# Optimization experiments

Measured on AMD Instinct MI355X. Metric: run time of the kernel, lower is better.

The kernel has to match this reference:

```python
import jax, jax.numpy as jnp
import numpy as np

N, M, D = 1024, 32, 512


def setup_inputs() -> dict:
    key = jax.random.key(0)
    k1, = jax.random.split(key, 1)
    emb = jax.random.normal(k1, (N, M, D), dtype=jnp.float32)
    emb = emb / jnp.linalg.norm(emb, axis=-1, keepdims=True)  # module expects normed embeddings
    return {
        "normed_embedding": emb,
        "n": N,
        "m": M,
        "ln_w": jnp.array(10.0, dtype=jnp.float32),
        "ln_b": jnp.array(-5.0, dtype=jnp.float32),
    }


def reference(normed_embedding, n, m, ln_w, ln_b):
    # normed_embedding: [N, M, D]
    ck = jnp.mean(normed_embedding, axis=1)          # [N, D] inclusive centroids
    sums = jnp.sum(normed_embedding, axis=1)         # [N, D]
    e = normed_embedding.reshape(n * m, -1)          # [NM, D]
    sims = jnp.matmul(e, ck.T)                       # [NM, N]

    # exclusive centroid for own speaker: cj = (sum_i - e_ij) / (m - 1)
    ex = jnp.sum(normed_embedding * (sums[:, None, :] - normed_embedding), axis=-1) / (m - 1)  # [N, M]
    rows = jnp.arange(n * m)
    spk = rows // m                                  # speaker label per row
    sims = sims.at[rows, spk].set(ex.reshape(-1))

    sims = jax.nn.sigmoid(ln_w * sims + ln_b)

    own = sims[rows, spk]                            # [NM]
    own_col = spk[:, None] == jnp.arange(n)[None, :]  # mask own speaker column
    max_other = jnp.max(jnp.where(own_col, -jnp.inf, sims), axis=-1)  # [NM]
    loss = jnp.mean(1.0 - own + max_other).reshape(1)

    preds = jnp.argmax(sims, axis=1)
    batch_acc = jnp.mean((preds == spk).astype(jnp.float32))
    return loss, batch_acc
```

## Files before the change

kernel.cpp:

```cpp
#include <hip/hip_runtime.h>


#define N_SPK 1024
#define M_UTT 32
#define D_DIM 512
#define NROWS (N_SPK * M_UTT)
#define BM 256
#define BN 256
#define NTILES (N_SPK / BN)
#define MTILES (NROWS / BM)
#define NWG (MTILES * NTILES)

typedef __attribute__((ext_vector_type(8))) short short8v;
typedef __attribute__((ext_vector_type(4))) float f32x4;

__device__ __forceinline__ unsigned short f2bf(float f) {
    union { float f; unsigned int u; } v; v.f = f;
    unsigned int u = v.u;
    u += 0x7fffu + ((u >> 16) & 1u);
    return (unsigned short)(u >> 16);
}

__device__ __forceinline__ void gload_lds16(const void* g, void* l) {
    __builtin_amdgcn_global_load_lds(
        (const __attribute__((address_space(1))) unsigned int*)g,
        (__attribute__((address_space(3))) unsigned int*)l, 16, 0, 0);
}

__device__ __forceinline__ float sigmoidf(float x) {
    return 1.f / (1.f + __expf(-x));
}

template <int MH, int NH>
__device__ __forceinline__ void qmm(f32x4 (&acc)[8][4],
                                    const short8v (&a)[4][2],
                                    const short8v (&b)[2][2]) {
#pragma unroll
    for (int mf = 0; mf < 4; ++mf)
#pragma unroll
        for (int nf = 0; nf < 2; ++nf) {
            acc[MH * 4 + mf][NH * 2 + nf] = __builtin_amdgcn_mfma_f32_16x16x32_bf16(
                a[mf][0], b[nf][0], acc[MH * 4 + mf][NH * 2 + nf], 0, 0, 0);
            acc[MH * 4 + mf][NH * 2 + nf] = __builtin_amdgcn_mfma_f32_16x16x32_bf16(
                a[mf][1], b[nf][1], acc[MH * 4 + mf][NH * 2 + nf], 0, 0, 0);
        }
}

__global__ void __launch_bounds__(256) prep_kernel(const float* __restrict__ emb,
                                                   const float* __restrict__ lnw,
                                                   unsigned short* __restrict__ ebf,
                                                   unsigned short* __restrict__ ck) {
    __shared__ float part[2][D_DIM];
    const int n = blockIdx.x;
    const int t = threadIdx.x;
    const int d4 = (t & 127) * 4;
    const int mh = t >> 7;
    const float* base = emb + (size_t)n * M_UTT * D_DIM;
    unsigned short* obase = ebf + (size_t)n * M_UTT * D_DIM;

    float4 acc = {0.f, 0.f, 0.f, 0.f};
#pragma unroll
    for (int mm = 0; mm < 16; ++mm) {
        const int m = mh * 16 + mm;
        const float4 v = *reinterpret_cast<const float4*>(base + m * D_DIM + d4);
        acc.x += v.x; acc.y += v.y; acc.z += v.z; acc.w += v.w;
        ushort4 b;
        b.x = f2bf(v.x); b.y = f2bf(v.y); b.z = f2bf(v.z); b.w = f2bf(v.w);
        *reinterpret_cast<ushort4*>(obase + m * D_DIM + d4) = b;
    }
    *reinterpret_cast<float4*>(&part[mh][d4]) = acc;
    __syncthreads();
    if (t < 128) {
        const float sgn = (lnw[0] >= 0.f) ? 1.f : -1.f;
        const float sc = sgn * (1.f / 32.f);
        const int d = t * 4;
        const float4 a = *reinterpret_cast<const float4*>(&part[0][d]);
        const float4 b = *reinterpret_cast<const float4*>(&part[1][d]);
        ushort4 o;
        o.x = f2bf((a.x + b.x) * sc); o.y = f2bf((a.y + b.y) * sc);
        o.z = f2bf((a.z + b.z) * sc); o.w = f2bf((a.w + b.w) * sc);
        *reinterpret_cast<ushort4*>(ck + (size_t)n * D_DIM + d) = o;
    }
}

__global__ void __launch_bounds__(512, 2)
gemm_kernel(const unsigned short* __restrict__ ebf,
            const unsigned short* __restrict__ ck,
            float* __restrict__ maxo_part,
            float* __restrict__ own_part) {
    __shared__ __align__(16) unsigned short ring[2][32768];

    const int tid  = threadIdx.x;
    const int lane = tid & 63;
    const int wv   = tid >> 6;
    const int lo   = lane & 15;
    const int hi   = lane >> 4;
    const int wm   = wv >> 2;
    const int wn   = wv & 3;

    const int raw   = blockIdx.x;
    const int xcd   = raw & 7;
    const int local = raw >> 3;
    const int mt    = xcd * 16 + (local >> 2);
    const int nt    = local & 3;
    const int r0    = mt * BM;
    const int n0    = nt * BN;

    const unsigned short* pA[2];
    const unsigned short* pB[2];
    int doff[2];
#pragma unroll
    for (int j = 0; j < 2; ++j) {
        const int s   = j * 512 + tid;
        const int row = s >> 3;
        const int l   = (s & 7) ^ (row & 7);
        pA[j] = ebf + (size_t)(r0 + row) * D_DIM + l * 8;
        pB[j] = ck  + (size_t)(n0 + row) * D_DIM + l * 8;
        doff[j] = s * 8;
    }

    auto stage_h = [&](int tile, int h) {
        unsigned short* dst = &ring[tile & 1][0];
        const int off = tile * 64 + h * (128 * D_DIM);
#pragma unroll
        for (int j = 0; j < 2; ++j) {
            gload_lds16(pA[j] + off, dst + h * 8192 + doff[j]);
            gload_lds16(pB[j] + off, dst + 16384 + h * 8192 + doff[j]);
        }
    };

    stage_h(0, 0);
    stage_h(0, 1);
    stage_h(1, 0);
    asm volatile("s_waitcnt vmcnt(4)" ::: "memory");
    __builtin_amdgcn_s_barrier();
    __builtin_amdgcn_sched_barrier(0);

    const int ph0   = (hi ^ (lo & 7)) * 16;
    const int ph1   = ((4 + hi) ^ (lo & 7)) * 16;
    const int arow0 = (wm * 128 + lo) * 128;
    const int bcol0 = 32768 + (wn * 64 + lo) * 128;

    f32x4 acc[8][4];
#pragma unroll
    for (int am = 0; am < 8; ++am)
#pragma unroll
        for (int an = 0; an < 4; ++an) acc[am][an] = (f32x4){0.f, 0.f, 0.f, 0.f};

    short8v a[4][2], b0c[2][2], b1c[2][2];

    for (int t = 0; t < 8; ++t) {
        const char* bufp = (const char*)&ring[t & 1][0];

#pragma unroll
        for (int mf = 0; mf < 4; ++mf) {
            a[mf][0] = *reinterpret_cast<const short8v*>(bufp + arow0 + mf * 2048 + ph0);
            a[mf][1] = *reinterpret_cast<const short8v*>(bufp + arow0 + mf * 2048 + ph1);
        }
#pragma unroll
        for (int nf = 0; nf < 2; ++nf) {
            b0c[nf][0] = *reinterpret_cast<const short8v*>(bufp + bcol0 + nf * 2048 + ph0);
            b0c[nf][1] = *reinterpret_cast<const short8v*>(bufp + bcol0 + nf * 2048 + ph1);
        }
        if (t < 7) stage_h(t + 1, 1);
        __builtin_amdgcn_s_barrier();
        __builtin_amdgcn_s_setprio(1);
        qmm<0, 0>(acc, a, b0c);
        __builtin_amdgcn_s_setprio(0);
        __builtin_amdgcn_s_barrier();

#pragma unroll
        for (int nf = 0; nf < 2; ++nf) {
            b1c[nf][0] = *reinterpret_cast<const short8v*>(bufp + bcol0 + 4096 + nf * 2048 + ph0);
            b1c[nf][1] = *reinterpret_cast<const short8v*>(bufp + bcol0 + 4096 + nf * 2048 + ph1);
        }
        __builtin_amdgcn_s_barrier();
        __builtin_amdgcn_s_setprio(1);
        qmm<0, 1>(acc, a, b1c);
        __builtin_amdgcn_s_setprio(0);
        __builtin_amdgcn_s_barrier();

#pragma unroll
        for (int mf = 0; mf < 4; ++mf) {
            a[mf][0] = *reinterpret_cast<const short8v*>(bufp + arow0 + 8192 + mf * 2048 + ph0);
            a[mf][1] = *reinterpret_cast<const short8v*>(bufp + arow0 + 8192 + mf * 2048 + ph1);
        }
        __builtin_amdgcn_s_barrier();
        __builtin_amdgcn_s_setprio(1);
        qmm<1, 1>(acc, a, b1c);
        __builtin_amdgcn_s_setprio(0);
        __builtin_amdgcn_s_barrier();

        if (t < 6) stage_h(t + 2, 0);
        __builtin_amdgcn_s_barrier();
        __builtin_amdgcn_s_setprio(1);
        qmm<1, 0>(acc, a, b0c);
        __builtin_amdgcn_s_setprio(0);
        if (t < 6)       asm volatile("s_waitcnt vmcnt(4)" ::: "memory");
        else if (t == 6) asm volatile("s_waitcnt vmcnt(0)" ::: "memory");
        __builtin_amdgcn_s_barrier();
        __builtin_amdgcn_sched_barrier(0);
    }

    __syncthreads();
    float* red = (float*)&ring[0][0];
    const float NEG = -1e30f;

#pragma unroll
    for (int am = 0; am < 8; ++am) {
#pragma unroll
        for (int reg = 0; reg < 4; ++reg) {
            const int rl   = wm * 128 + am * 16 + hi * 4 + reg;
            const int rowg = r0 + rl;
            const int spk  = rowg >> 5;
            float m = NEG, o = NEG;
#pragma unroll
            for (int an = 0; an < 4; ++an) {
                const int col = n0 + wn * 64 + an * 16 + lo;
                const float v = acc[am][an][reg];
                const bool dg = (col == spk);
                o = dg ? v : o;
                m = fmaxf(m, dg ? NEG : v);
            }
#pragma unroll
            for (int mask = 1; mask < 16; mask <<= 1) {
                m = fmaxf(m, __shfl_xor(m, mask));
                o = fmaxf(o, __shfl_xor(o, mask));
            }
            if (lo == 0) {
                red[wn * 256 + rl]        = m;
                red[1024 + wn * 256 + rl] = o;
            }
        }
    }
    __syncthreads();

    if (tid < 256) {
        const float mo = fmaxf(fmaxf(red[tid], red[256 + tid]),
                               fmaxf(red[512 + tid], red[768 + tid]));
        maxo_part[(size_t)nt * NROWS + r0 + tid] = mo;
        if (nt == (mt >> 5)) {
            const float op = fmaxf(fmaxf(red[1024 + tid], red[1280 + tid]),
                                   fmaxf(red[1536 + tid], red[1792 + tid]));
            own_part[r0 + tid] = op;
        }
    }
}

__global__ void __launch_bounds__(256) rowred_kernel(const float* __restrict__ maxo_part,
                                                     const float* __restrict__ own_part,
                                                     const float* __restrict__ lnw,
                                                     const float* __restrict__ lnb,
                                                     float* __restrict__ partsum) {
    const int r = blockIdx.x * 256 + threadIdx.x;
    const float lw = lnw[0], lb = lnb[0];
    const float sgn = (lw >= 0.f) ? 1.f : -1.f;
    const float alw = fabsf(lw);

    float mo = maxo_part[r];
#pragma unroll
    for (int nt2 = 1; nt2 < NTILES; ++nt2)
        mo = fmaxf(mo, maxo_part[(size_t)nt2 * NROWS + r]);
    const float ownp  = own_part[r];
    const float s_own = sgn * ownp;
    const float ex    = (32.f * s_own - 1.f) * (1.f / 31.f);
    const float own_s = sigmoidf(lw * ex + lb);
    const float mo_s  = sigmoidf(alw * mo + lb);
    float loss = 1.f - own_s + mo_s;
    float corr = (sgn * ex >= mo) ? 1.f : 0.f;

#pragma unroll
    for (int mask = 1; mask < 64; mask <<= 1) {
        loss += __shfl_xor(loss, mask);
        corr += __shfl_xor(corr, mask);
    }
    __shared__ float sl[4], sc[4];
    const int wv = threadIdx.x >> 6;
    if ((threadIdx.x & 63) == 0) { sl[wv] = loss; sc[wv] = corr; }
    __syncthreads();
    if (threadIdx.x == 0) {
        partsum[blockIdx.x]       = sl[0] + sl[1] + sl[2] + sl[3];
        partsum[128 + blockIdx.x] = sc[0] + sc[1] + sc[2] + sc[3];
    }
}

__global__ void __launch_bounds__(128) final_kernel(const float* __restrict__ partsum,
                                                    float* __restrict__ out) {
    const int t = threadIdx.x;
    float l = partsum[t];
    float c = partsum[128 + t];
#pragma unroll
    for (int mask = 1; mask < 64; mask <<= 1) {
        l += __shfl_xor(l, mask);
        c += __shfl_xor(c, mask);
    }
    __shared__ float sl[2], sc[2];
    if ((t & 63) == 0) { sl[t >> 6] = l; sc[t >> 6] = c; }
    __syncthreads();
    if (t == 0) {
        out[0] = (sl[0] + sl[1]) * (1.f / (float)NROWS);
        out[1] = (sc[0] + sc[1]) * (1.f / (float)NROWS);
    }
}

extern "C" void kernel_launch(void* const* d_in, const int* in_sizes, int n_in,
                              void* d_out, int out_size, void* d_ws, size_t ws_size,
                              hipStream_t stream) {
    (void)in_sizes; (void)n_in; (void)out_size; (void)ws_size;
    const float* emb = (const float*)d_in[0];
    const float* lnw = (const float*)d_in[3];
    const float* lnb = (const float*)d_in[4];
    float* out = (float*)d_out;

    char* ws = (char*)d_ws;
    unsigned short* ebf = (unsigned short*)ws;
    unsigned short* ck  = (unsigned short*)(ws + (size_t)NROWS * D_DIM * 2);
    float* maxo_part = (float*)(ws + (size_t)NROWS * D_DIM * 2
                                   + (size_t)N_SPK * D_DIM * 2);
    float* own_part  = (float*)((char*)maxo_part + (size_t)NTILES * NROWS * 4);
    float* partsum   = (float*)((char*)own_part + (size_t)NROWS * 4);

    prep_kernel<<<N_SPK, 256, 0, stream>>>(emb, lnw, ebf, ck);
    gemm_kernel<<<NWG, 512, 0, stream>>>(ebf, ck, maxo_part, own_part);
    rowred_kernel<<<NROWS / 256, 256, 0, stream>>>(maxo_part, own_part, lnw, lnb, partsum);
    final_kernel<<<1, 128, 0, stream>>>(partsum, out);
}
```

Measured before the change: 66.36 us.

## Fuse bf16 conversion of embeddings into GEMM loader and process two row panels per block

The prep kernel no longer writes a bf16 copy of the embeddings. The GEMM now loads fp32 embeddings through registers, truncates them to bf16, and stores them into LDS. Each workgroup covers 512 rows as two 256-row panels, keeping the centroid B tiles streamed, with half as many workgroups. This removes the extra global write and reread of the bf16 copy, at the cost of register-staged loads, more VALU packing work, fewer blocks (256 on the device), and truncation instead of round-to-nearest for A.

After: 81.93 us. 1.23x slower.

```diff
diff --git a/kernel.cpp b/kernel.cpp
--- a/kernel.cpp
+++ b/kernel.cpp
@@ -5,14 +5,12 @@
 #define M_UTT 32
 #define D_DIM 512
 #define NROWS (N_SPK * M_UTT)
-#define BM 256
-#define BN 256
-#define NTILES (N_SPK / BN)
-#define MTILES (NROWS / BM)
-#define NWG (MTILES * NTILES)
+#define NTILES 4
+#define GRID_G 256
 
 typedef __attribute__((ext_vector_type(8))) short short8v;
 typedef __attribute__((ext_vector_type(4))) float f32x4;
+typedef __attribute__((ext_vector_type(4))) unsigned int u32x4;
 
 __device__ __forceinline__ unsigned short f2bf(float f) {
     union { float f; unsigned int u; } v; v.f = f;
@@ -21,6 +19,11 @@
     return (unsigned short)(u >> 16);
 }
 
+__device__ __forceinline__ unsigned int pk2(float a, float b) {
+    union { float f; unsigned int u; } ua, ub; ua.f = a; ub.f = b;
+    return (ub.u & 0xFFFF0000u) | (ua.u >> 16);
+}
+
 __device__ __forceinline__ void gload_lds16(const void* g, void* l) {
     __builtin_amdgcn_global_load_lds(
         (const __attribute__((address_space(1))) unsigned int*)g,
@@ -46,17 +49,15 @@
         }
 }
 
-__global__ void __launch_bounds__(256) prep_kernel(const float* __restrict__ emb,
-                                                   const float* __restrict__ lnw,
-                                                   unsigned short* __restrict__ ebf,
-                                                   unsigned short* __restrict__ ck) {
+__global__ void __launch_bounds__(256) ck_kernel(const float* __restrict__ emb,
+                                                 const float* __restrict__ lnw,
+                                                 unsigned short* __restrict__ ck) {
     __shared__ float part[2][D_DIM];
     const int n = blockIdx.x;
     const int t = threadIdx.x;
     const int d4 = (t & 127) * 4;
     const int mh = t >> 7;
     const float* base = emb + (size_t)n * M_UTT * D_DIM;
-    unsigned short* obase = ebf + (size_t)n * M_UTT * D_DIM;
 
     float4 acc = {0.f, 0.f, 0.f, 0.f};
 #pragma unroll
@@ -64,9 +65,6 @@
         const int m = mh * 16 + mm;
         const float4 v = *reinterpret_cast<const float4*>(base + m * D_DIM + d4);
         acc.x += v.x; acc.y += v.y; acc.z += v.z; acc.w += v.w;
-        ushort4 b;
-        b.x = f2bf(v.x); b.y = f2bf(v.y); b.z = f2bf(v.z); b.w = f2bf(v.w);
-        *reinterpret_cast<ushort4*>(obase + m * D_DIM + d4) = b;
     }
     *reinterpret_cast<float4*>(&part[mh][d4]) = acc;
     __syncthreads();
@@ -84,11 +82,12 @@
 }
 
 __global__ void __launch_bounds__(512, 2)
-gemm_kernel(const unsigned short* __restrict__ ebf,
+gemm_kernel(const float* __restrict__ emb,
             const unsigned short* __restrict__ ck,
             float* __restrict__ maxo_part,
             float* __restrict__ own_part) {
-    __shared__ __align__(16) unsigned short ring[2][32768];
+    __shared__ __align__(16) unsigned short buf[2][32768];
+    __shared__ float red[2][2][4][256];
 
     const int tid  = threadIdx.x;
     const int lane = tid & 63;
@@ -99,150 +98,206 @@
     const int wn   = wv & 3;
 
     const int raw   = blockIdx.x;
-    const int xcd   = raw & 7;
-    const int local = raw >> 3;
-    const int mt    = xcd * 16 + (local >> 2);
-    const int nt    = local & 3;
-    const int r0    = mt * BM;
-    const int n0    = nt * BN;
-
-    const unsigned short* pA[2];
-    const unsigned short* pB[2];
-    int doff[2];
+    const int P     = (raw & 7) * 8 + ((raw >> 3) >> 2);
+    const int ntb   = (raw >> 3) & 3;
+    const int r0    = P * 512;
+    const int n0    = ntb * 256;
+
+    const int lsw = (tid & 7) ^ ((tid >> 3) & 7);
+    const unsigned aoff0 = (unsigned)(r0 + (tid >> 3)) * 512u + (unsigned)lsw * 8u;
+    const unsigned boff0 = (unsigned)(n0 + (tid >> 3)) * 512u + (unsigned)lsw * 8u;
+    const int dA = tid * 8;
+    const int dB = 16384 + tid * 8;
+
+    const int ph0   = (hi ^ (lo & 7)) * 8;
+    const int ph1   = ((4 + hi) ^ (lo & 7)) * 8;
+    const int abase = (wm * 128 + lo) * 64;
+    const int bbase = 16384 + (wn * 64 + lo) * 64;
+
+    float4 ga[4], gb[4];
+
 #pragma unroll
     for (int j = 0; j < 2; ++j) {
-        const int s   = j * 512 + tid;
-        const int row = s >> 3;
-        const int l   = (s & 7) ^ (row & 7);
-        pA[j] = ebf + (size_t)(r0 + row) * D_DIM + l * 8;
-        pB[j] = ck  + (size_t)(n0 + row) * D_DIM + l * 8;
-        doff[j] = s * 8;
-    }
-
-    auto stage_h = [&](int tile, int h) {
-        unsigned short* dst = &ring[tile & 1][0];
-        const int off = tile * 64 + h * (128 * D_DIM);
-#pragma unroll
-        for (int j = 0; j < 2; ++j) {
-            gload_lds16(pA[j] + off, dst + h * 8192 + doff[j]);
-            gload_lds16(pB[j] + off, dst + 16384 + h * 8192 + doff[j]);
-        }
-    };
-
-    stage_h(0, 0);
-    stage_h(0, 1);
-    stage_h(1, 0);
+        ga[2 * j]     = *reinterpret_cast<const float4*>(emb + aoff0 + j * 32768u);
+        ga[2 * j + 1] = *reinterpret_cast<const float4*>(emb + aoff0 + j * 32768u + 4u);
+        gb[2 * j]     = *reinterpret_cast<const float4*>(emb + aoff0 + (j + 2) * 32768u);
+        gb[2 * j + 1] = *reinterpret_cast<const float4*>(emb + aoff0 + (j + 2) * 32768u + 4u);
+    }
+#pragma unroll
+    for (int j = 0; j < 4; ++j)
+        gload_lds16(ck + boff0 + j * 32768u, &buf[0][dB + j * 4096]);
+#pragma unroll
+    for (int j = 0; j < 4; ++j)
+        gload_lds16(ck + boff0 + j * 32768u + 64u, &buf[1][dB + j * 4096]);
+    {
+        u32x4 w0 = {pk2(ga[0].x, ga[0].y), pk2(ga[0].z, ga[0].w),
+                    pk2(ga[1].x, ga[1].y), pk2(ga[1].z, ga[1].w)};
+        u32x4 w1 = {pk2(ga[2].x, ga[2].y), pk2(ga[2].z, ga[2].w),
+                    pk2(ga[3].x, ga[3].y), pk2(ga[3].z, ga[3].w)};
+        u32x4 w2 = {pk2(gb[0].x, gb[0].y), pk2(gb[0].z, gb[0].w),
+                    pk2(gb[1].x, gb[1].y), pk2(gb[1].z, gb[1].w)};
+        u32x4 w3 = {pk2(gb[2].x, gb[2].y), pk2(gb[2].z, gb[2].w),
+                    pk2(gb[3].x, gb[3].y), pk2(gb[3].z, gb[3].w)};
+        *reinterpret_cast<u32x4*>(&buf[0][dA])         = w0;
+        *reinterpret_cast<u32x4*>(&buf[0][dA + 4096])  = w1;
+        *reinterpret_cast<u32x4*>(&buf[0][dA + 8192])  = w2;
+        *reinterpret_cast<u32x4*>(&buf[0][dA + 12288]) = w3;
+    }
+    asm volatile("s_waitcnt lgkmcnt(0)" ::: "memory");
     asm volatile("s_waitcnt vmcnt(4)" ::: "memory");
     __builtin_amdgcn_s_barrier();
     __builtin_amdgcn_sched_barrier(0);
 
-    const int ph0   = (hi ^ (lo & 7)) * 16;
-    const int ph1   = ((4 + hi) ^ (lo & 7)) * 16;
-    const int arow0 = (wm * 128 + lo) * 128;
-    const int bcol0 = 32768 + (wn * 64 + lo) * 128;
-
     f32x4 acc[8][4];
 #pragma unroll
     for (int am = 0; am < 8; ++am)
 #pragma unroll
         for (int an = 0; an < 4; ++an) acc[am][an] = (f32x4){0.f, 0.f, 0.f, 0.f};
 
-    short8v a[4][2], b0c[2][2], b1c[2][2];
-
-    for (int t = 0; t < 8; ++t) {
-        const char* bufp = (const char*)&ring[t & 1][0];
-
+    short8v afr[4][2], b0c[2][2], b1c[2][2];
+    const float NEG = -1e30f;
+
+#pragma unroll
+    for (int tau = 0; tau < 16; ++tau) {
+        const int cur = tau & 1;
+        const unsigned short* bp  = &buf[cur][0];
+        unsigned short*       bpn = &buf[cur ^ 1][0];
+        const unsigned kA = (unsigned)((((tau + 1) >> 3) * 131072) + (((tau + 1) & 7) * 64));
+        const unsigned kB = (unsigned)(((tau + 2) & 7) * 64);
+
+        if (tau < 15) {
+#pragma unroll
+            for (int j = 0; j < 2; ++j) {
+                ga[2 * j]     = *reinterpret_cast<const float4*>(emb + aoff0 + kA + j * 32768u);
+                ga[2 * j + 1] = *reinterpret_cast<const float4*>(emb + aoff0 + kA + j * 32768u + 4u);
+            }
+        }
 #pragma unroll
         for (int mf = 0; mf < 4; ++mf) {
-            a[mf][0] = *reinterpret_cast<const short8v*>(bufp + arow0 + mf * 2048 + ph0);
-            a[mf][1] = *reinterpret_cast<const short8v*>(bufp + arow0 + mf * 2048 + ph1);
+            afr[mf][0] = *reinterpret_cast<const short8v*>(bp + abase + mf * 1024 + ph0);
+            afr[mf][1] = *reinterpret_cast<const short8v*>(bp + abase + mf * 1024 + ph1);
         }
 #pragma unroll
         for (int nf = 0; nf < 2; ++nf) {
-            b0c[nf][0] = *reinterpret_cast<const short8v*>(bufp + bcol0 + nf * 2048 + ph0);
-            b0c[nf][1] = *reinterpret_cast<const short8v*>(bufp + bcol0 + nf * 2048 + ph1);
-        }
-        if (t < 7) stage_h(t + 1, 1);
+            b0c[nf][0] = *reinterpret_cast<const short8v*>(bp + bbase + nf * 1024 + ph0);
+            b0c[nf][1] = *reinterpret_cast<const short8v*>(bp + bbase + nf * 1024 + ph1);
+        }
         __builtin_amdgcn_s_barrier();
         __builtin_amdgcn_s_setprio(1);
-        qmm<0, 0>(acc, a, b0c);
+        qmm<0, 0>(acc, afr, b0c);
         __builtin_amdgcn_s_setprio(0);
         __builtin_amdgcn_s_barrier();
 
+        if (tau < 15) {
+#pragma unroll
+            for (int j = 0; j < 2; ++j) {
+                gb[2 * j]     = *reinterpret_cast<const float4*>(emb + aoff0 + kA + (j + 2) * 32768u);
+                gb[2 * j + 1] = *reinterpret_cast<const float4*>(emb + aoff0 + kA + (j + 2) * 32768u + 4u);
+            }
+        }
 #pragma unroll
         for (int nf = 0; nf < 2; ++nf) {
-            b1c[nf][0] = *reinterpret_cast<const short8v*>(bufp + bcol0 + 4096 + nf * 2048 + ph0);
-            b1c[nf][1] = *reinterpret_cast<const short8v*>(bufp + bcol0 + 4096 + nf * 2048 + ph1);
+            b1c[nf][0] = *reinterpret_cast<const short8v*>(bp + bbase + 2048 + nf * 1024 + ph0);
+            b1c[nf][1] = *reinterpret_cast<const short8v*>(bp + bbase + 2048 + nf * 1024 + ph1);
         }
         __builtin_amdgcn_s_barrier();
         __builtin_amdgcn_s_setprio(1);
-        qmm<0, 1>(acc, a, b1c);
+        qmm<0, 1>(acc, afr, b1c);
         __builtin_amdgcn_s_setprio(0);
         __builtin_amdgcn_s_barrier();
 
+        if (tau < 14) {
+#pragma unroll
+            for (int j = 0; j < 4; ++j)
+                gload_lds16(ck + boff0 + kB + j * 32768u, &buf[cur][dB + j * 4096]);
+        }
+        if (tau < 15) {
+            u32x4 w0 = {pk2(ga[0].x, ga[0].y), pk2(ga[0].z, ga[0].w),
+                        pk2(ga[1].x, ga[1].y), pk2(ga[1].z, ga[1].w)};
+            u32x4 w1 = {pk2(ga[2].x, ga[2].y), pk2(ga[2].z, ga[2].w),
+                        pk2(ga[3].x, ga[3].y), pk2(ga[3].z, ga[3].w)};
+            *reinterpret_cast<u32x4*>(bpn + dA)        = w0;
+            *reinterpret_cast<u32x4*>(bpn + dA + 4096) = w1;
+        }
 #pragma unroll
         for (int mf = 0; mf < 4; ++mf) {
-            a[mf][0] = *reinterpret_cast<const short8v*>(bufp + arow0 + 8192 + mf * 2048 + ph0);
-            a[mf][1] = *reinterpret_cast<const short8v*>(bufp + arow0 + 8192 + mf * 2048 + ph1);
+            afr[mf][0] = *reinterpret_cast<const short8v*>(bp + abase + 4096 + mf * 1024 + ph0);
+            afr[mf][1] = *reinterpret_cast<const short8v*>(bp + abase + 4096 + mf * 1024 + ph1);
         }
         __builtin_amdgcn_s_barrier();
         __builtin_amdgcn_s_setprio(1);
-        qmm<1, 1>(acc, a, b1c);
+        qmm<1, 1>(acc, afr, b1c);
         __builtin_amdgcn_s_setprio(0);
         __builtin_amdgcn_s_barrier();
 
-        if (t < 6) stage_h(t + 2, 0);
+        if (tau < 15) {
+            u32x4 w2 = {pk2(gb[0].x, gb[0].y), pk2(gb[0].z, gb[0].w),
+                        pk2(gb[1].x, gb[1].y), pk2(gb[1].z, gb[1].w)};
+            u32x4 w3 = {pk2(gb[2].x, gb[2].y), pk2(gb[2].z, gb[2].w),
+                        pk2(gb[3].x, gb[3].y), pk2(gb[3].z, gb[3].w)};
+            *reinterpret_cast<u32x4*>(bpn + dA + 8192)  = w2;
+            *reinterpret_cast<u32x4*>(bpn + dA + 12288) = w3;
+        }
+        asm volatile("s_waitcnt lgkmcnt(0)" ::: "memory");
         __builtin_amdgcn_s_barrier();
         __builtin_amdgcn_s_setprio(1);
-        qmm<1, 0>(acc, a, b0c);
+        qmm<1, 0>(acc, afr, b0c);
         __builtin_amdgcn_s_setprio(0);
-        if (t < 6)       asm volatile("s_waitcnt vmcnt(4)" ::: "memory");
-        else if (t == 6) asm volatile("s_waitcnt vmcnt(0)" ::: "memory");
         __builtin_amdgcn_s_barrier();
         __builtin_amdgcn_sched_barrier(0);
+
+        if (tau == 7 || tau == 15) {
+            const int pan = tau >> 3;
+#pragma unroll
+            for (int am = 0; am < 8; ++am) {
+#pragma unroll
+                for (int reg = 0; reg < 4; ++reg) {
+                    const int rl   = wm * 128 + am * 16 + hi * 4 + reg;
+                    const int rowg = r0 + pan * 256 + rl;
+                    const int spk  = rowg >> 5;
+                    float m = NEG, o = NEG;
+#pragma unroll
+                    for (int an = 0; an < 4; ++an) {
+                        const int col = n0 + wn * 64 + an * 16 + lo;
+                        const float v = acc[am][an][reg];
+                        const bool dg = (col == spk);
+                        o = dg ? v : o;
+                        m = fmaxf(m, dg ? NEG : v);
+                    }
+#pragma unroll
+                    for (int mask = 1; mask < 16; mask <<= 1) {
+                        m = fmaxf(m, __shfl_xor(m, mask));
+                        o = fmaxf(o, __shfl_xor(o, mask));
+                    }
+                    if (lo == 0) {
+                        red[pan][0][wn][rl] = m;
+                        red[pan][1][wn][rl] = o;
+                    }
+                }
+            }
+            if (tau == 7) {
+#pragma unroll
+                for (int am = 0; am < 8; ++am)
+#pragma unroll
+                    for (int an = 0; an < 4; ++an)
+                        acc[am][an] = (f32x4){0.f, 0.f, 0.f, 0.f};
+            }
+        }
     }
 
     __syncthreads();
-    float* red = (float*)&ring[0][0];
-    const float NEG = -1e30f;
-
-#pragma unroll
-    for (int am = 0; am < 8; ++am) {
-#pragma unroll
-        for (int reg = 0; reg < 4; ++reg) {
-            const int rl   = wm * 128 + am * 16 + hi * 4 + reg;
-            const int rowg = r0 + rl;
-            const int spk  = rowg >> 5;
-            float m = NEG, o = NEG;
-#pragma unroll
-            for (int an = 0; an < 4; ++an) {
-                const int col = n0 + wn * 64 + an * 16 + lo;
-                const float v = acc[am][an][reg];
-                const bool dg = (col == spk);
-                o = dg ? v : o;
-                m = fmaxf(m, dg ? NEG : v);
-            }
-#pragma unroll
-            for (int mask = 1; mask < 16; mask <<= 1) {
-                m = fmaxf(m, __shfl_xor(m, mask));
-                o = fmaxf(o, __shfl_xor(o, mask));
-            }
-            if (lo == 0) {
-                red[wn * 256 + rl]        = m;
-                red[1024 + wn * 256 + rl] = o;
-            }
-        }
-    }
-    __syncthreads();
-
     if (tid < 256) {
-        const float mo = fmaxf(fmaxf(red[tid], red[256 + tid]),
-                               fmaxf(red[512 + tid], red[768 + tid]));
-        maxo_part[(size_t)nt * NROWS + r0 + tid] = mo;
-        if (nt == (mt >> 5)) {
-            const float op = fmaxf(fmaxf(red[1024 + tid], red[1280 + tid]),
-                                   fmaxf(red[1536 + tid], red[1792 + tid]));
-            own_part[r0 + tid] = op;
+#pragma unroll
+        for (int pan = 0; pan < 2; ++pan) {
+            const float mo = fmaxf(fmaxf(red[pan][0][0][tid], red[pan][0][1][tid]),
+                                   fmaxf(red[pan][0][2][tid], red[pan][0][3][tid]));
+            maxo_part[(size_t)ntb * NROWS + r0 + pan * 256 + tid] = mo;
+            const int mtp = P * 2 + pan;
+            if (ntb == (mtp >> 5)) {
+                const float op = fmaxf(fmaxf(red[pan][1][0][tid], red[pan][1][1][tid]),
+                                       fmaxf(red[pan][1][2][tid], red[pan][1][3][tid]));
+                own_part[r0 + pan * 256 + tid] = op;
+            }
         }
     }
 }
@@ -313,15 +368,13 @@
     float* out = (float*)d_out;
 
     char* ws = (char*)d_ws;
-    unsigned short* ebf = (unsigned short*)ws;
-    unsigned short* ck  = (unsigned short*)(ws + (size_t)NROWS * D_DIM * 2);
-    float* maxo_part = (float*)(ws + (size_t)NROWS * D_DIM * 2
-                                   + (size_t)N_SPK * D_DIM * 2);
+    unsigned short* ck = (unsigned short*)ws;
+    float* maxo_part = (float*)(ws + (size_t)N_SPK * D_DIM * 2);
     float* own_part  = (float*)((char*)maxo_part + (size_t)NTILES * NROWS * 4);
     float* partsum   = (float*)((char*)own_part + (size_t)NROWS * 4);
 
-    prep_kernel<<<N_SPK, 256, 0, stream>>>(emb, lnw, ebf, ck);
-    gemm_kernel<<<NWG, 512, 0, stream>>>(ebf, ck, maxo_part, own_part);
+    ck_kernel<<<N_SPK, 256, 0, stream>>>(emb, lnw, ck);
+    gemm_kernel<<<GRID_G, 512, 0, stream>>>(emb, ck, maxo_part, own_part);
     rowred_kernel<<<NROWS / 256, 256, 0, stream>>>(maxo_part, own_part, lnw, lnb, partsum);
     final_kernel<<<1, 128, 0, stream>>>(partsum, out);
 }
```

## Make GEMM workgroups sweep two column tiles, halving grid and partials

Applied to the files above, without the earlier changes.

Each GEMM workgroup now walks two consecutive 256-column speaker tiles (16 K-steps in one pipelined loop) instead of one. Row max and own-speaker values are folded into registers at each tile boundary and the accumulators reset. The grid drops from 512 to 256 workgroups, so each A row-tile is loaded by two workgroups instead of four and only two maxo partials go to rowred. The cost is extra register pressure from the mx/ow arrays and the fully unrolled loop, plus fewer workgroups to fill the CUs (256 CUs on MI355X, one wave of launches).

After: 82.75 us. +24.7%, slower.

```diff
diff --git a/kernel.cpp b/kernel.cpp
--- a/kernel.cpp
+++ b/kernel.cpp
@@ -6,10 +6,9 @@
 #define D_DIM 512
 #define NROWS (N_SPK * M_UTT)
 #define BM 256
-#define BN 256
-#define NTILES (N_SPK / BN)
-#define MTILES (NROWS / BM)
-#define NWG (MTILES * NTILES)
+#define NPARTS 2
+#define GRID_G 256
+#define NKT 16
 
 typedef __attribute__((ext_vector_type(8))) short short8v;
 typedef __attribute__((ext_vector_type(4))) float f32x4;
@@ -101,10 +100,10 @@
     const int raw   = blockIdx.x;
     const int xcd   = raw & 7;
     const int local = raw >> 3;
-    const int mt    = xcd * 16 + (local >> 2);
-    const int nt    = local & 3;
+    const int mt    = xcd * 16 + (local & 15);
+    const int ch    = local >> 4;
     const int r0    = mt * BM;
-    const int n0    = nt * BN;
+    const int c0    = ch * 512;
 
     const unsigned short* pA[2];
     const unsigned short* pB[2];
@@ -115,17 +114,18 @@
         const int row = s >> 3;
         const int l   = (s & 7) ^ (row & 7);
         pA[j] = ebf + (size_t)(r0 + row) * D_DIM + l * 8;
-        pB[j] = ck  + (size_t)(n0 + row) * D_DIM + l * 8;
+        pB[j] = ck  + (size_t)(c0 + row) * D_DIM + l * 8;
         doff[j] = s * 8;
     }
 
     auto stage_h = [&](int tile, int h) {
         unsigned short* dst = &ring[tile & 1][0];
-        const int off = tile * 64 + h * (128 * D_DIM);
+        const int offA = (tile & 7) * 64 + h * (128 * D_DIM);
+        const int offB = offA + ((tile >> 3) << 17);
 #pragma unroll
         for (int j = 0; j < 2; ++j) {
-            gload_lds16(pA[j] + off, dst + h * 8192 + doff[j]);
-            gload_lds16(pB[j] + off, dst + 16384 + h * 8192 + doff[j]);
+            gload_lds16(pA[j] + offA, dst + h * 8192 + doff[j]);
+            gload_lds16(pB[j] + offB, dst + 16384 + h * 8192 + doff[j]);
         }
     };
 
@@ -142,14 +142,21 @@
     const int bcol0 = 32768 + (wn * 64 + lo) * 128;
 
     f32x4 acc[8][4];
+    float mx[8][4], ow[8][4];
+    const float NEG = -1e30f;
 #pragma unroll
     for (int am = 0; am < 8; ++am)
 #pragma unroll
         for (int an = 0; an < 4; ++an) acc[am][an] = (f32x4){0.f, 0.f, 0.f, 0.f};
+#pragma unroll
+    for (int am = 0; am < 8; ++am)
+#pragma unroll
+        for (int reg = 0; reg < 4; ++reg) { mx[am][reg] = NEG; ow[am][reg] = NEG; }
 
     short8v a[4][2], b0c[2][2], b1c[2][2];
 
-    for (int t = 0; t < 8; ++t) {
+#pragma unroll
+    for (int t = 0; t < NKT; ++t) {
         const char* bufp = (const char*)&ring[t & 1][0];
 
 #pragma unroll
@@ -162,7 +169,7 @@
             b0c[nf][0] = *reinterpret_cast<const short8v*>(bufp + bcol0 + nf * 2048 + ph0);
             b0c[nf][1] = *reinterpret_cast<const short8v*>(bufp + bcol0 + nf * 2048 + ph1);
         }
-        if (t < 7) stage_h(t + 1, 1);
+        if (t < NKT - 1) stage_h(t + 1, 1);
         __builtin_amdgcn_s_barrier();
         __builtin_amdgcn_s_setprio(1);
         qmm<0, 0>(acc, a, b0c);
@@ -191,43 +198,58 @@
         __builtin_amdgcn_s_setprio(0);
         __builtin_amdgcn_s_barrier();
 
-        if (t < 6) stage_h(t + 2, 0);
+        if (t < NKT - 2) stage_h(t + 2, 0);
         __builtin_amdgcn_s_barrier();
         __builtin_amdgcn_s_setprio(1);
         qmm<1, 0>(acc, a, b0c);
         __builtin_amdgcn_s_setprio(0);
-        if (t < 6)       asm volatile("s_waitcnt vmcnt(4)" ::: "memory");
-        else if (t == 6) asm volatile("s_waitcnt vmcnt(0)" ::: "memory");
+        if (t < NKT - 2)       asm volatile("s_waitcnt vmcnt(4)" ::: "memory");
+        else if (t == NKT - 2) asm volatile("s_waitcnt vmcnt(0)" ::: "memory");
         __builtin_amdgcn_s_barrier();
         __builtin_amdgcn_sched_barrier(0);
+
+        if (t == 7 || t == 15) {
+            const int ntl = t >> 3;
+#pragma unroll
+            for (int am = 0; am < 8; ++am)
+#pragma unroll
+                for (int reg = 0; reg < 4; ++reg) {
+                    const int rowg = r0 + wm * 128 + am * 16 + hi * 4 + reg;
+                    const int spk  = rowg >> 5;
+#pragma unroll
+                    for (int an = 0; an < 4; ++an) {
+                        const int col = c0 + ntl * 256 + wn * 64 + an * 16 + lo;
+                        const float v = acc[am][an][reg];
+                        const bool dg = (col == spk);
+                        ow[am][reg] = dg ? v : ow[am][reg];
+                        mx[am][reg] = fmaxf(mx[am][reg], dg ? NEG : v);
+                    }
+                }
+            if (t == 7) {
+#pragma unroll
+                for (int am = 0; am < 8; ++am)
+#pragma unroll
+                    for (int an = 0; an < 4; ++an)
+                        acc[am][an] = (f32x4){0.f, 0.f, 0.f, 0.f};
+            }
+        }
     }
 
     __syncthreads();
     float* red = (float*)&ring[0][0];
-    const float NEG = -1e30f;
 
 #pragma unroll
     for (int am = 0; am < 8; ++am) {
 #pragma unroll
         for (int reg = 0; reg < 4; ++reg) {
-            const int rl   = wm * 128 + am * 16 + hi * 4 + reg;
-            const int rowg = r0 + rl;
-            const int spk  = rowg >> 5;
-            float m = NEG, o = NEG;
-#pragma unroll
-            for (int an = 0; an < 4; ++an) {
-                const int col = n0 + wn * 64 + an * 16 + lo;
-                const float v = acc[am][an][reg];
-                const bool dg = (col == spk);
-                o = dg ? v : o;
-                m = fmaxf(m, dg ? NEG : v);
-            }
+            float m = mx[am][reg], o = ow[am][reg];
 #pragma unroll
             for (int mask = 1; mask < 16; mask <<= 1) {
                 m = fmaxf(m, __shfl_xor(m, mask));
                 o = fmaxf(o, __shfl_xor(o, mask));
             }
             if (lo == 0) {
+                const int rl = wm * 128 + am * 16 + hi * 4 + reg;
                 red[wn * 256 + rl]        = m;
                 red[1024 + wn * 256 + rl] = o;
             }
@@ -238,8 +260,8 @@
     if (tid < 256) {
         const float mo = fmaxf(fmaxf(red[tid], red[256 + tid]),
                                fmaxf(red[512 + tid], red[768 + tid]));
-        maxo_part[(size_t)nt * NROWS + r0 + tid] = mo;
-        if (nt == (mt >> 5)) {
+        maxo_part[(size_t)ch * NROWS + r0 + tid] = mo;
+        if (ch == (mt >> 6)) {
             const float op = fmaxf(fmaxf(red[1024 + tid], red[1280 + tid]),
                                    fmaxf(red[1536 + tid], red[1792 + tid]));
             own_part[r0 + tid] = op;
@@ -257,10 +279,7 @@
     const float sgn = (lw >= 0.f) ? 1.f : -1.f;
     const float alw = fabsf(lw);
 
-    float mo = maxo_part[r];
-#pragma unroll
-    for (int nt2 = 1; nt2 < NTILES; ++nt2)
-        mo = fmaxf(mo, maxo_part[(size_t)nt2 * NROWS + r]);
+    const float mo = fmaxf(maxo_part[r], maxo_part[(size_t)NROWS + r]);
     const float ownp  = own_part[r];
     const float s_own = sgn * ownp;
     const float ex    = (32.f * s_own - 1.f) * (1.f / 31.f);
@@ -317,11 +336,11 @@
     unsigned short* ck  = (unsigned short*)(ws + (size_t)NROWS * D_DIM * 2);
     float* maxo_part = (float*)(ws + (size_t)NROWS * D_DIM * 2
                                    + (size_t)N_SPK * D_DIM * 2);
-    float* own_part  = (float*)((char*)maxo_part + (size_t)NTILES * NROWS * 4);
+    float* own_part  = (float*)((char*)maxo_part + (size_t)NPARTS * NROWS * 4);
     float* partsum   = (float*)((char*)own_part + (size_t)NROWS * 4);
 
     prep_kernel<<<N_SPK, 256, 0, stream>>>(emb, lnw, ebf, ck);
-    gemm_kernel<<<NWG, 512, 0, stream>>>(ebf, ck, maxo_part, own_part);
+    gemm_kernel<<<GRID_G, 512, 0, stream>>>(ebf, ck, maxo_part, own_part);
     rowred_kernel<<<NROWS / 256, 256, 0, stream>>>(maxo_part, own_part, lnw, lnb, partsum);
     final_kernel<<<1, 128, 0, stream>>>(partsum, out);
 }
```
